# Kernel optimization log

Hardware: AMD Instinct MI355X
Metric: run time of the kernel (lower is better)

The kernel has to match this reference:

```python
import jax, jax.numpy as jnp
import numpy as np

N = 50000      # nodes
E = 800000     # edges (avg degree 16)
F_IN = 128     # input feature dim
HID = 128      # 2 * out_classes
OUT = 64       # out_classes


def setup_inputs() -> dict:
    key = jax.random.key(0)
    ks = jax.random.split(key, 12)
    x = jax.random.normal(ks[0], (N, F_IN), jnp.float32)
    edge_index = jax.random.randint(ks[1], (2, E), 0, N, jnp.int32)
    def lin(k, fi, fo):
        return jax.random.normal(k, (fi, fo), jnp.float32) / np.float32(np.sqrt(fi))
    return {
        "x": x,
        "edge_index": edge_index,
        "W1": lin(ks[2], F_IN, HID), "b1": jnp.zeros((HID,), jnp.float32),
        "W2": lin(ks[3], HID, HID),  "b2": jnp.zeros((HID,), jnp.float32),
        "W3": lin(ks[4], HID, HID),  "b3": jnp.zeros((HID,), jnp.float32),
        "jk_w": jax.random.normal(ks[5], (3,), jnp.float32),
        "fc_W": lin(ks[6], HID, OUT), "fc_b": jnp.zeros((OUT,), jnp.float32),
    }


def _gcn_conv(h, W, b, row, col, n):
    """PyG GCNConv: linear -> add self-loops -> sym-normalized aggregate -> bias."""
    h = h @ W                                        # [n, d_out]
    loops = jnp.arange(n, dtype=row.dtype)
    r = jnp.concatenate([row, loops])                # sources
    c = jnp.concatenate([col, loops])                # targets
    deg = jax.ops.segment_sum(jnp.ones_like(c, h.dtype), c, num_segments=n)
    dinv = jnp.where(deg > 0, jax.lax.rsqrt(deg), 0.0)
    norm = dinv[r] * dinv[c]                         # [E+n]
    msg = h[r] * norm[:, None]                       # gather + scale
    return jax.ops.segment_sum(msg, c, num_segments=n) + b


def _neighbor_mean(h, row, col, n):
    """sample_neighbors with scale_factor=2: exact mean over out-neighbors,
    own feature when degree == 0 (top-k branch is provably dead code)."""
    s = jax.ops.segment_sum(h[col], row, num_segments=n)
    deg = jax.ops.segment_sum(jnp.ones_like(row, h.dtype), row, num_segments=n)
    mean = s / jnp.maximum(deg, 1.0)[:, None]
    return jnp.where((deg > 0)[:, None], mean, h)


def reference(x, edge_index, W1, b1, W2, b2, W3, b3, jk_w, fc_W, fc_b):
    row, col = edge_index[0], edge_index[1]
    n = x.shape[0]
    # layer 0: GCN -> ReLU -> (dropout: eval identity) -> neighbor sampling
    h0 = jax.nn.relu(_gcn_conv(x, W1, b1, row, col, n))
    h0 = _neighbor_mean(h0, row, col, n)
    # layer 1: GCN -> ReLU; historical-activation update is identity on first call
    h1 = jax.nn.relu(_gcn_conv(h0, W2, b2, row, col, n))
    # layer 2
    h2 = jax.nn.relu(_gcn_conv(h1, W3, b3, row, col, n))
    # dynamic JK aggregation
    w = jax.nn.softmax(jk_w)
    h = w[0] * h0 + w[1] * h1 + w[2] * h2
    return h @ fc_W + fc_b
```

## Files before the change

kernel.cpp:

```cpp
#include <hip/hip_runtime.h>
#include <stdint.h>

typedef unsigned int  uint32;
typedef unsigned short u16;

typedef short bfx8 __attribute__((ext_vector_type(8)));
typedef float f32x4 __attribute__((ext_vector_type(4)));
typedef float f32x2 __attribute__((ext_vector_type(2)));

#define NBP 256
#define CH  2048

__device__ __forceinline__ float b2f(u16 u) {
    union { uint32 i; float f; } v; v.i = ((uint32)u) << 16; return v.f;
}
__device__ __forceinline__ u16 f2b(float f) {
    union { float f; uint32 i; } v; v.f = f;
    uint32 u = v.i;
    return (u16)((u + 0x7fffu + ((u >> 16) & 1u)) >> 16);
}
__device__ __forceinline__ float blo(uint32 u) {
    union { uint32 i; float f; } v; v.i = u << 16; return v.f;
}
__device__ __forceinline__ float bhi(uint32 u) {
    union { uint32 i; float f; } v; v.i = u & 0xffff0000u; return v.f;
}
__device__ __forceinline__ uint32 packbf(float a, float b) {
    return (uint32)f2b(a) | ((uint32)f2b(b) << 16);
}
__device__ __forceinline__ void splitf(float x, u16& h, u16& l) {
    h = f2b(x);
    l = f2b(x - b2f(h));
}
__device__ __forceinline__ void split8(const float* __restrict__ p, bfx8& hi, bfx8& lo) {
    f32x4 a = *(const f32x4*)p;
    f32x4 b = *(const f32x4*)(p + 4);
    float x[8] = {a[0], a[1], a[2], a[3], b[0], b[1], b[2], b[3]};
#pragma unroll
    for (int j = 0; j < 8; ++j) {
        u16 h, l; splitf(x[j], h, l);
        hi[j] = (short)h; lo[j] = (short)l;
    }
}

__global__ __launch_bounds__(256) void k_preA(
    const int* __restrict__ row, const int* __restrict__ col, int E, int Gh,
    int* __restrict__ cntC, int* __restrict__ cntR,
    const float* __restrict__ W1, const float* __restrict__ W2,
    const float* __restrict__ W3, const float* __restrict__ fcW,
    u16* __restrict__ WTh, u16* __restrict__ WTl, int WTN) {
    if ((int)blockIdx.x < Gh) {
        __shared__ int hp[NBP];
        int t = threadIdx.x;
        hp[t] = 0;
        __syncthreads();
        int base = blockIdx.x * CH;
        int n = E - base; if (n > CH) n = CH;
        for (int i = t; i < n; i += 256) {
            int r = row[base + i], c = col[base + i];
            atomicAdd(&hp[c >> 8], 1);
            atomicAdd(&hp[r >> 8], 0x10000);
        }
        __syncthreads();
        int v = hp[t];
        if (v & 0xffff) atomicAdd(&cntC[t], v & 0xffff);
        if (v >> 16)    atomicAdd(&cntR[t], v >> 16);
        return;
    }
    int i = ((int)blockIdx.x - Gh) * 256 + threadIdx.x;
    if (i >= WTN) return;
    float w;
    if (i < 3 * 16384) {
        int m = i >> 14, j = i & 16383;
        int fo = j >> 7, fi = j & 127;
        const float* W = (m == 0) ? W1 : (m == 1) ? W2 : W3;
        w = W[fi * 128 + fo];
    } else {
        int j = i - 3 * 16384;
        int fo = j >> 7, fi = j & 127;
        w = fcW[fi * 64 + fo];
    }
    u16 h, l; splitf(w, h, l);
    WTh[i] = h; WTl[i] = l;
}

__global__ __launch_bounds__(256) void k_scanB(
    const int* __restrict__ cntC, const int* __restrict__ cntR,
    int* __restrict__ bOffC, int* __restrict__ bOffR,
    int* __restrict__ curC, int* __restrict__ curR, int NB) {
    int t = threadIdx.x;
    int lane = t & 63, wid = t >> 6;
    __shared__ int wsum[4];
    for (int m = 0; m < 2; ++m) {
        const int* cnt = m ? cntR : cntC;
        int* bOff = m ? bOffR : bOffC;
        int* cur  = m ? curR  : curC;
        int v = (t < NB) ? cnt[t] : 0;
        int x = v;
#pragma unroll
        for (int d = 1; d < 64; d <<= 1) {
            int u = __shfl_up(x, d);
            if (lane >= d) x += u;
        }
        if (lane == 63) wsum[wid] = x;
        __syncthreads();
        int add = 0;
        for (int i = 0; i < wid; ++i) add += wsum[i];
        int ex = x + add - v;
        if (t <= NB) bOff[t] = ex;
        cur[t] = ex;
        __syncthreads();
    }
}

__device__ __forceinline__ void gemm128_f32_body(
    const float* __restrict__ A, const u16* __restrict__ WTh, const u16* __restrict__ WTl,
    const float* __restrict__ dinv, u16* __restrict__ G, int M, int blk) {
    const int lane = threadIdx.x & 63;
    const int q = lane >> 4, l = lane & 15;
    int rbase = blk * 128 + (threadIdx.x >> 6) * 32;
    if (rbase >= M) return;
    int r0 = rbase + l;      if (r0 >= M) r0 = M - 1;
    int r1 = rbase + 16 + l; if (r1 >= M) r1 = M - 1;

    f32x4 acc[2][8];
#pragma unroll
    for (int i = 0; i < 2; ++i)
#pragma unroll
        for (int j = 0; j < 8; ++j) acc[i][j] = (f32x4){0.f, 0.f, 0.f, 0.f};

#pragma unroll
    for (int kc = 0; kc < 4; ++kc) {
        int k0 = kc * 32 + q * 8;
        bfx8 ah0, al0, ah1, al1;
        split8(A + (size_t)r0 * 128 + k0, ah0, al0);
        split8(A + (size_t)r1 * 128 + k0, ah1, al1);
#pragma unroll
        for (int ct = 0; ct < 8; ++ct) {
            bfx8 bh = *(const bfx8*)(WTh + (ct * 16 + l) * 128 + k0);
            bfx8 bl = *(const bfx8*)(WTl + (ct * 16 + l) * 128 + k0);
            acc[0][ct] = __builtin_amdgcn_mfma_f32_16x16x32_bf16(ah0, bh, acc[0][ct], 0, 0, 0);
            acc[0][ct] = __builtin_amdgcn_mfma_f32_16x16x32_bf16(ah0, bl, acc[0][ct], 0, 0, 0);
            acc[0][ct] = __builtin_amdgcn_mfma_f32_16x16x32_bf16(al0, bh, acc[0][ct], 0, 0, 0);
            acc[1][ct] = __builtin_amdgcn_mfma_f32_16x16x32_bf16(ah1, bh, acc[1][ct], 0, 0, 0);
            acc[1][ct] = __builtin_amdgcn_mfma_f32_16x16x32_bf16(ah1, bl, acc[1][ct], 0, 0, 0);
            acc[1][ct] = __builtin_amdgcn_mfma_f32_16x16x32_bf16(al1, bh, acc[1][ct], 0, 0, 0);
        }
    }
#pragma unroll
    for (int rs = 0; rs < 2; ++rs) {
#pragma unroll
        for (int rr = 0; rr < 4; ++rr) {
            int rw = rbase + rs * 16 + q * 4 + rr;
            if (rw < M) {
                float dv = dinv ? dinv[rw] : 1.0f;
#pragma unroll
                for (int ct = 0; ct < 8; ++ct)
                    G[(size_t)rw * 128 + ct * 16 + l] = f2b(acc[rs][ct][rr] * dv);
            }
        }
    }
}

__global__ __launch_bounds__(256) void k_gemm0(
    const float* __restrict__ A, const u16* __restrict__ WTh, const u16* __restrict__ WTl,
    u16* __restrict__ G, int M) {
    gemm128_f32_body(A, WTh, WTl, nullptr, G, M, blockIdx.x);
}

__global__ __launch_bounds__(256) void k_gemm128_pl(
    const u16* __restrict__ Ah, const u16* __restrict__ Al,
    const u16* __restrict__ WTh, const u16* __restrict__ WTl,
    const float* __restrict__ dinv, u16* __restrict__ G, int M) {
    const int lane = threadIdx.x & 63;
    const int q = lane >> 4, l = lane & 15;
    int rbase = blockIdx.x * 128 + (threadIdx.x >> 6) * 32;
    if (rbase >= M) return;
    int r0 = rbase + l;      if (r0 >= M) r0 = M - 1;
    int r1 = rbase + 16 + l; if (r1 >= M) r1 = M - 1;

    f32x4 acc[2][8];
#pragma unroll
    for (int i = 0; i < 2; ++i)
#pragma unroll
        for (int j = 0; j < 8; ++j) acc[i][j] = (f32x4){0.f, 0.f, 0.f, 0.f};

#pragma unroll
    for (int kc = 0; kc < 4; ++kc) {
        int k0 = kc * 32 + q * 8;
        bfx8 ah0 = *(const bfx8*)(Ah + (size_t)r0 * 128 + k0);
        bfx8 al0 = *(const bfx8*)(Al + (size_t)r0 * 128 + k0);
        bfx8 ah1 = *(const bfx8*)(Ah + (size_t)r1 * 128 + k0);
        bfx8 al1 = *(const bfx8*)(Al + (size_t)r1 * 128 + k0);
#pragma unroll
        for (int ct = 0; ct < 8; ++ct) {
            bfx8 bh = *(const bfx8*)(WTh + (ct * 16 + l) * 128 + k0);
            bfx8 bl = *(const bfx8*)(WTl + (ct * 16 + l) * 128 + k0);
            acc[0][ct] = __builtin_amdgcn_mfma_f32_16x16x32_bf16(ah0, bh, acc[0][ct], 0, 0, 0);
            acc[0][ct] = __builtin_amdgcn_mfma_f32_16x16x32_bf16(ah0, bl, acc[0][ct], 0, 0, 0);
            acc[0][ct] = __builtin_amdgcn_mfma_f32_16x16x32_bf16(al0, bh, acc[0][ct], 0, 0, 0);
            acc[1][ct] = __builtin_amdgcn_mfma_f32_16x16x32_bf16(ah1, bh, acc[1][ct], 0, 0, 0);
            acc[1][ct] = __builtin_amdgcn_mfma_f32_16x16x32_bf16(ah1, bl, acc[1][ct], 0, 0, 0);
            acc[1][ct] = __builtin_amdgcn_mfma_f32_16x16x32_bf16(al1, bh, acc[1][ct], 0, 0, 0);
        }
    }
#pragma unroll
    for (int rs = 0; rs < 2; ++rs) {
#pragma unroll
        for (int rr = 0; rr < 4; ++rr) {
            int rw = rbase + rs * 16 + q * 4 + rr;
            if (rw < M) {
                float dv = dinv[rw];
#pragma unroll
                for (int ct = 0; ct < 8; ++ct)
                    G[(size_t)rw * 128 + ct * 16 + l] = f2b(acc[rs][ct][rr] * dv);
            }
        }
    }
}

__global__ __launch_bounds__(256) void k_partC(
    const int* __restrict__ row, const int* __restrict__ col, int E,
    int* __restrict__ curC, int* __restrict__ curR,
    uint32* __restrict__ partC, uint32* __restrict__ partR) {
    __shared__ uint32 stagedC[CH], stagedR[CH];
    __shared__ int hp[NBP], expk[NBP], curp[NBP], runC[NBP], runR[NBP];
    __shared__ int wsum[4];
    int t = threadIdx.x;
    int lane = t & 63, wid = t >> 6;
    int base = blockIdx.x * CH;
    int n = E - base; if (n > CH) n = CH;

    int er[8], ec[8];
#pragma unroll
    for (int j = 0; j < 8; ++j) {
        int i = t + j * 256;
        if (i < n) { er[j] = row[base + i]; ec[j] = col[base + i]; }
        else er[j] = -1;
    }
    hp[t] = 0;
    __syncthreads();
#pragma unroll
    for (int j = 0; j < 8; ++j) {
        if (er[j] >= 0) {
            atomicAdd(&hp[ec[j] >> 8], 1);
            atomicAdd(&hp[er[j] >> 8], 0x10000);
        }
    }
    __syncthreads();
    int v = hp[t];
    int x = v;
#pragma unroll
    for (int d = 1; d < 64; d <<= 1) {
        int u = __shfl_up(x, d);
        if (lane >= d) x += u;
    }
    if (lane == 63) wsum[wid] = x;
    __syncthreads();
    int add = 0;
    for (int i = 0; i < wid; ++i) add += wsum[i];
    int ex = x + add - v;
    expk[t] = ex;
    curp[t] = ex;
    int vC = v & 0xffff, vR = v >> 16;
    runC[t] = vC ? atomicAdd(&curC[t], vC) : 0;
    runR[t] = vR ? atomicAdd(&curR[t], vR) : 0;
    __syncthreads();
#pragma unroll
    for (int j = 0; j < 8; ++j) {
        if (er[j] >= 0) {
            int cb = ec[j] >> 8, rb = er[j] >> 8;
            int pC = atomicAdd(&curp[cb], 1) & 0xffff;
            stagedC[pC] = ((uint32)ec[j] << 16) | (uint32)er[j];
            int pR = atomicAdd(&curp[rb], 0x10000) >> 16;
            stagedR[pR] = ((uint32)er[j] << 16) | (uint32)ec[j];
        }
    }
    __syncthreads();
    for (int i = t; i < n; i += 256) {
        uint32 pv = stagedC[i];
        int b = pv >> 24;
        partC[runC[b] + (i - (expk[b] & 0xffff))] = pv;
    }
    for (int i = t; i < n; i += 256) {
        uint32 pv = stagedR[i];
        int b = pv >> 24;
        partR[runR[b] + (i - (expk[b] >> 16))] = pv;
    }
}

__global__ __launch_bounds__(256) void k_fillD(
    const uint32* __restrict__ partC, const uint32* __restrict__ partR,
    const int* __restrict__ bOffC, const int* __restrict__ bOffR,
    int* __restrict__ off_in, int* __restrict__ off_out,
    u16* __restrict__ csr_src, u16* __restrict__ csr_dst,
    float* __restrict__ dinv, int NB, int N, int E) {
    int part = ((int)blockIdx.x >= NB) ? 1 : 0;
    int b = (int)blockIdx.x - part * NB;
    const uint32* arr = part ? partR : partC;
    const int* bOff   = part ? bOffR : bOffC;
    int* offA         = part ? off_out : off_in;
    u16* csr          = part ? csr_dst : csr_src;
    int t = threadIdx.x;
    int lane = t & 63, wid = t >> 6;
    int base = bOff[b], end = bOff[b + 1];
    __shared__ int cnt[NBP], cur[NBP];
    __shared__ int wsum[4];
    cnt[t] = 0;
    __syncthreads();
    for (int i = base + t; i < end; i += 256)
        atomicAdd(&cnt[(arr[i] >> 16) & 255], 1);
    __syncthreads();
    int v = cnt[t];
    int x = v;
#pragma unroll
    for (int d = 1; d < 64; d <<= 1) {
        int u = __shfl_up(x, d);
        if (lane >= d) x += u;
    }
    if (lane == 63) wsum[wid] = x;
    __syncthreads();
    int add = 0;
    for (int i = 0; i < wid; ++i) add += wsum[i];
    int ex = x + add - v;
    cur[t] = ex;
    int node = (b << 8) + t;
    if (node < N) {
        offA[node] = base + ex;
        if (part == 0) dinv[node] = rsqrtf((float)(v + 1));
    }
    if (b == 0 && t == 0) offA[N] = E;
    __syncthreads();
    for (int i = base + t; i < end; i += 256) {
        uint32 pv = arr[i];
        int local = (pv >> 16) & 255;
        int pos = atomicAdd(&cur[local], 1);
        csr[base + pos] = (u16)(pv & 0xffffu);
    }
}

template <int MODE>
__global__ __launch_bounds__(256) void k_agg(
    const uint32* __restrict__ g, const u16* __restrict__ csr_src,
    const int* __restrict__ off, const float* __restrict__ dinv,
    const f32x2* __restrict__ bias, uint32* __restrict__ outH,
    uint32* __restrict__ outL, int n) {
    int w = (blockIdx.x * 256 + threadIdx.x) >> 6;
    if (w >= n) return;
    int lane = threadIdx.x & 63;
    float dc = dinv[w];
    uint32 sv = g[(size_t)w * 64 + lane];
    float s0, s1;
    if (MODE == 0) { s0 = blo(sv) * dc; s1 = bhi(sv) * dc; }
    else           { s0 = blo(sv);      s1 = bhi(sv); }
    int e = off[w], e1 = off[w + 1];
    for (; e + 8 <= e1; e += 8) {
        int ix[8];
#pragma unroll
        for (int j = 0; j < 8; ++j) ix[j] = csr_src[e + j];
        uint32 vv[8];
#pragma unroll
        for (int j = 0; j < 8; ++j) vv[j] = g[(size_t)ix[j] * 64 + lane];
        if (MODE == 0) {
            float dm[8];
#pragma unroll
            for (int j = 0; j < 8; ++j) dm[j] = dinv[ix[j]];
#pragma unroll
            for (int j = 0; j < 8; ++j) {
                s0 = fmaf(blo(vv[j]), dm[j], s0);
                s1 = fmaf(bhi(vv[j]), dm[j], s1);
            }
        } else {
#pragma unroll
            for (int j = 0; j < 8; ++j) { s0 += blo(vv[j]); s1 += bhi(vv[j]); }
        }
    }
    for (; e < e1; ++e) {
        int ix = csr_src[e];
        uint32 v = g[(size_t)ix * 64 + lane];
        if (MODE == 0) {
            float dm = dinv[ix];
            s0 = fmaf(blo(v), dm, s0);
            s1 = fmaf(bhi(v), dm, s1);
        } else {
            s0 += blo(v); s1 += bhi(v);
        }
    }
    f32x2 bb = bias[lane];
    float o0 = fmaxf(fmaf(s0, dc, bb[0]), 0.f);
    float o1 = fmaxf(fmaf(s1, dc, bb[1]), 0.f);
    if (MODE == 0) {
        outH[(size_t)w * 64 + lane] = packbf(o0, o1);
    } else {
        u16 h0, l0, h1, l1;
        splitf(o0, h0, l0);
        splitf(o1, h1, l1);
        outH[(size_t)w * 64 + lane] = (uint32)h0 | ((uint32)h1 << 16);
        outL[(size_t)w * 64 + lane] = (uint32)l0 | ((uint32)l1 << 16);
    }
}

__global__ __launch_bounds__(256) void k_mean(
    const uint32* __restrict__ h, const u16* __restrict__ csr_dst,
    const int* __restrict__ off, uint32* __restrict__ outH,
    uint32* __restrict__ outL, int n) {
    int w = (blockIdx.x * 256 + threadIdx.x) >> 6;
    if (w >= n) return;
    int lane = threadIdx.x & 63;
    int e = off[w], e1 = off[w + 1];
    int d = e1 - e;
    float s0 = 0.f, s1 = 0.f;
    for (; e + 8 <= e1; e += 8) {
        int ix[8];
#pragma unroll
        for (int j = 0; j < 8; ++j) ix[j] = csr_dst[e + j];
        uint32 vv[8];
#pragma unroll
        for (int j = 0; j < 8; ++j) vv[j] = h[(size_t)ix[j] * 64 + lane];
#pragma unroll
        for (int j = 0; j < 8; ++j) { s0 += blo(vv[j]); s1 += bhi(vv[j]); }
    }
    for (; e < e1; ++e) {
        uint32 v = h[(size_t)csr_dst[e] * 64 + lane];
        s0 += blo(v); s1 += bhi(v);
    }
    float o0, o1;
    if (d > 0) {
        float inv = 1.f / (float)d;
        o0 = s0 * inv; o1 = s1 * inv;
    } else {
        uint32 sv = h[(size_t)w * 64 + lane];
        o0 = blo(sv); o1 = bhi(sv);
    }
    u16 ha, la, hb, lb;
    splitf(o0, ha, la);
    splitf(o1, hb, lb);
    outH[(size_t)w * 64 + lane] = (uint32)ha | ((uint32)hb << 16);
    outL[(size_t)w * 64 + lane] = (uint32)la | ((uint32)lb << 16);
}

__global__ __launch_bounds__(256) void k_final(
    const u16* __restrict__ h0h, const u16* __restrict__ h0l,
    const u16* __restrict__ h1h, const u16* __restrict__ h1l,
    const u16* __restrict__ h2h, const u16* __restrict__ h2l,
    const float* __restrict__ jkw,
    const u16* __restrict__ fcWTh, const u16* __restrict__ fcWTl,
    const float* __restrict__ fcb, float* __restrict__ out, int M) {
    float a0 = jkw[0], a1 = jkw[1], a2 = jkw[2];
    float mx = fmaxf(a0, fmaxf(a1, a2));
    float e0 = expf(a0 - mx), e1 = expf(a1 - mx), e2 = expf(a2 - mx);
    float inv = 1.f / (e0 + e1 + e2);
    float w0 = e0 * inv, w1 = e1 * inv, w2 = e2 * inv;

    const int lane = threadIdx.x & 63;
    const int q = lane >> 4, l = lane & 15;
    int rbase = blockIdx.x * 128 + (threadIdx.x >> 6) * 32;
    if (rbase >= M) return;
    int r0 = rbase + l;      if (r0 >= M) r0 = M - 1;
    int r1 = rbase + 16 + l; if (r1 >= M) r1 = M - 1;

    f32x4 acc[2][4];
#pragma unroll
    for (int i = 0; i < 2; ++i)
#pragma unroll
        for (int j = 0; j < 4; ++j) acc[i][j] = (f32x4){0.f, 0.f, 0.f, 0.f};

    union U8 { bfx8 v; u16 u[8]; };

#pragma unroll
    for (int kc = 0; kc < 4; ++kc) {
        int k0 = kc * 32 + q * 8;
        bfx8 ah[2], al[2];
        const int rr2[2] = {r0, r1};
#pragma unroll
        for (int half = 0; half < 2; ++half) {
            size_t o = (size_t)rr2[half] * 128 + k0;
            U8 x0h, x0l, x1h, x1l, x2h, x2l, rh, rl;
            x0h.v = *(const bfx8*)(h0h + o); x0l.v = *(const bfx8*)(h0l + o);
            x1h.v = *(const bfx8*)(h1h + o); x1l.v = *(const bfx8*)(h1l + o);
            x2h.v = *(const bfx8*)(h2h + o); x2l.v = *(const bfx8*)(h2l + o);
#pragma unroll
            for (int j = 0; j < 8; ++j) {
                float v0 = b2f(x0h.u[j]) + b2f(x0l.u[j]);
                float v1 = b2f(x1h.u[j]) + b2f(x1l.u[j]);
                float v2 = b2f(x2h.u[j]) + b2f(x2l.u[j]);
                float c = w0 * v0 + w1 * v1 + w2 * v2;
                u16 ch, cl; splitf(c, ch, cl);
                rh.u[j] = ch; rl.u[j] = cl;
            }
            ah[half] = rh.v; al[half] = rl.v;
        }
#pragma unroll
        for (int ct = 0; ct < 4; ++ct) {
            bfx8 bh = *(const bfx8*)(fcWTh + (ct * 16 + l) * 128 + k0);
            bfx8 bl = *(const bfx8*)(fcWTl + (ct * 16 + l) * 128 + k0);
#pragma unroll
            for (int half = 0; half < 2; ++half) {
                acc[half][ct] = __builtin_amdgcn_mfma_f32_16x16x32_bf16(ah[half], bh, acc[half][ct], 0, 0, 0);
                acc[half][ct] = __builtin_amdgcn_mfma_f32_16x16x32_bf16(ah[half], bl, acc[half][ct], 0, 0, 0);
                acc[half][ct] = __builtin_amdgcn_mfma_f32_16x16x32_bf16(al[half], bh, acc[half][ct], 0, 0, 0);
            }
        }
    }
#pragma unroll
    for (int rs = 0; rs < 2; ++rs) {
#pragma unroll
        for (int rr = 0; rr < 4; ++rr) {
            int rw = rbase + rs * 16 + q * 4 + rr;
            if (rw < M) {
#pragma unroll
                for (int ct = 0; ct < 4; ++ct) {
                    int cc = ct * 16 + l;
                    out[(size_t)rw * 64 + cc] = acc[rs][ct][rr] + fcb[cc];
                }
            }
        }
    }
}

extern "C" void kernel_launch(void* const* d_in, const int* in_sizes, int n_in,
                              void* d_out, int out_size, void* d_ws, size_t ws_size,
                              hipStream_t stream) {
    const int N = in_sizes[0] / 128;
    const int E = in_sizes[1] / 2;
    const int NB = (N + 255) >> 8;

    const float* x    = (const float*)d_in[0];
    const int* row    = (const int*)d_in[1];
    const int* col    = row + E;
    const float* W1   = (const float*)d_in[2];
    const float* b1   = (const float*)d_in[3];
    const float* W2   = (const float*)d_in[4];
    const float* b2   = (const float*)d_in[5];
    const float* W3   = (const float*)d_in[6];
    const float* b3   = (const float*)d_in[7];
    const float* jkw  = (const float*)d_in[8];
    const float* fcW  = (const float*)d_in[9];
    const float* fcb  = (const float*)d_in[10];
    float* outp       = (float*)d_out;

    char* ws = (char*)d_ws;
    size_t off = 0;
    auto alloc = [&](size_t bytes) -> char* {
        char* p = ws + off;
        off += (bytes + 255) & ~(size_t)255;
        return p;
    };
    int* cntC   = (int*)alloc((size_t)2 * NBP * sizeof(int));
    int* cntR   = cntC + NBP;
    int* bOffC  = (int*)alloc((size_t)(NBP + 1) * sizeof(int));
    int* bOffR  = (int*)alloc((size_t)(NBP + 1) * sizeof(int));
    int* curC   = (int*)alloc((size_t)NBP * sizeof(int));
    int* curR   = (int*)alloc((size_t)NBP * sizeof(int));
    int* off_in  = (int*)alloc((size_t)(N + 1) * sizeof(int));
    int* off_out = (int*)alloc((size_t)(N + 1) * sizeof(int));
    uint32* partC = (uint32*)alloc((size_t)E * sizeof(uint32));
    uint32* partR = (uint32*)alloc((size_t)E * sizeof(uint32));
    u16* csr_src = (u16*)alloc((size_t)E * sizeof(u16));
    u16* csr_dst = (u16*)alloc((size_t)E * sizeof(u16));
    float* dinv  = (float*)alloc((size_t)N * sizeof(float));
    const int WTN = 3 * 16384 + 8192;
    u16* WTh = (u16*)alloc((size_t)WTN * sizeof(u16));
    u16* WTl = (u16*)alloc((size_t)WTN * sizeof(u16));
    size_t FB = (size_t)N * 128 * sizeof(u16);
    u16* gbuf = (u16*)alloc(FB);
    u16* t0   = (u16*)alloc(FB);
    u16* h0h = (u16*)alloc(FB); u16* h0l = (u16*)alloc(FB);
    u16* h1h = (u16*)alloc(FB); u16* h1l = (u16*)alloc(FB);
    u16* h2h = (u16*)alloc(FB); u16* h2l = (u16*)alloc(FB);

    hipMemsetAsync(cntC, 0, (size_t)2 * NBP * sizeof(int), stream);

    const int B = 256;
    int Gh = (E + CH - 1) / CH;
    int Gwt = (WTN + B - 1) / B;
    int Gg = (N + 127) / 128;
    k_preA<<<Gh + Gwt, B, 0, stream>>>(row, col, E, Gh, cntC, cntR,
                                       W1, W2, W3, fcW, WTh, WTl, WTN);
    k_scanB<<<1, B, 0, stream>>>(cntC, cntR, bOffC, bOffR, curC, curR, NB);
    k_gemm0<<<Gg, B, 0, stream>>>(x, WTh, WTl, gbuf, N);
    k_partC<<<Gh, B, 0, stream>>>(row, col, E, curC, curR, partC, partR);
    k_fillD<<<2 * NB, B, 0, stream>>>(partC, partR, bOffC, bOffR,
                                      off_in, off_out, csr_src, csr_dst, dinv, NB, N, E);

    int aggG = (N + 3) / 4;

    k_agg<0><<<aggG, B, 0, stream>>>((const uint32*)gbuf, csr_src, off_in, dinv,
                                     (const f32x2*)b1, (uint32*)t0, nullptr, N);
    k_mean<<<aggG, B, 0, stream>>>((const uint32*)t0, csr_dst, off_out,
                                   (uint32*)h0h, (uint32*)h0l, N);
    k_gemm128_pl<<<Gg, B, 0, stream>>>(h0h, h0l, WTh + 16384, WTl + 16384, dinv, gbuf, N);
    k_agg<1><<<aggG, B, 0, stream>>>((const uint32*)gbuf, csr_src, off_in, dinv,
                                     (const f32x2*)b2, (uint32*)h1h, (uint32*)h1l, N);
    k_gemm128_pl<<<Gg, B, 0, stream>>>(h1h, h1l, WTh + 2 * 16384, WTl + 2 * 16384, dinv, gbuf, N);
    k_agg<1><<<aggG, B, 0, stream>>>((const uint32*)gbuf, csr_src, off_in, dinv,
                                     (const f32x2*)b3, (uint32*)h2h, (uint32*)h2l, N);
    k_final<<<Gg, B, 0, stream>>>(h0h, h0l, h1h, h1l, h2h, h2l, jkw,
                                  WTh + 3 * 16384, WTl + 3 * 16384, fcb, outp, N);
}
```

Measured before the change: 381.4 us.

## Drop hi/lo activation split, use fixed-capacity buckets, widen gather unroll

```diff
diff --git a/kernel.cpp b/kernel.cpp
--- a/kernel.cpp
+++ b/kernel.cpp
@@ -10,6 +10,7 @@
 
 #define NBP 256
 #define CH  2048
+#define BS  4608
 
 __device__ __forceinline__ float b2f(u16 u) {
     union { uint32 i; float f; } v; v.i = ((uint32)u) << 16; return v.f;
@@ -43,31 +44,18 @@
     }
 }
 
-__global__ __launch_bounds__(256) void k_preA(
-    const int* __restrict__ row, const int* __restrict__ col, int E, int Gh,
-    int* __restrict__ cntC, int* __restrict__ cntR,
+__global__ __launch_bounds__(256) void k_init(
+    int* __restrict__ curC, int* __restrict__ curR,
     const float* __restrict__ W1, const float* __restrict__ W2,
     const float* __restrict__ W3, const float* __restrict__ fcW,
     u16* __restrict__ WTh, u16* __restrict__ WTl, int WTN) {
-    if ((int)blockIdx.x < Gh) {
-        __shared__ int hp[NBP];
-        int t = threadIdx.x;
-        hp[t] = 0;
-        __syncthreads();
-        int base = blockIdx.x * CH;
-        int n = E - base; if (n > CH) n = CH;
-        for (int i = t; i < n; i += 256) {
-            int r = row[base + i], c = col[base + i];
-            atomicAdd(&hp[c >> 8], 1);
-            atomicAdd(&hp[r >> 8], 0x10000);
-        }
-        __syncthreads();
-        int v = hp[t];
-        if (v & 0xffff) atomicAdd(&cntC[t], v & 0xffff);
-        if (v >> 16)    atomicAdd(&cntR[t], v >> 16);
+    int t = threadIdx.x;
+    if (blockIdx.x == 0) {
+        curC[t] = t * BS;
+        curR[t] = t * BS;
         return;
     }
-    int i = ((int)blockIdx.x - Gh) * 256 + threadIdx.x;
+    int i = ((int)blockIdx.x - 1) * 256 + t;
     if (i >= WTN) return;
     float w;
     if (i < 3 * 16384) {
@@ -84,41 +72,12 @@
     WTh[i] = h; WTl[i] = l;
 }
 
-__global__ __launch_bounds__(256) void k_scanB(
-    const int* __restrict__ cntC, const int* __restrict__ cntR,
-    int* __restrict__ bOffC, int* __restrict__ bOffR,
-    int* __restrict__ curC, int* __restrict__ curR, int NB) {
-    int t = threadIdx.x;
-    int lane = t & 63, wid = t >> 6;
-    __shared__ int wsum[4];
-    for (int m = 0; m < 2; ++m) {
-        const int* cnt = m ? cntR : cntC;
-        int* bOff = m ? bOffR : bOffC;
-        int* cur  = m ? curR  : curC;
-        int v = (t < NB) ? cnt[t] : 0;
-        int x = v;
-#pragma unroll
-        for (int d = 1; d < 64; d <<= 1) {
-            int u = __shfl_up(x, d);
-            if (lane >= d) x += u;
-        }
-        if (lane == 63) wsum[wid] = x;
-        __syncthreads();
-        int add = 0;
-        for (int i = 0; i < wid; ++i) add += wsum[i];
-        int ex = x + add - v;
-        if (t <= NB) bOff[t] = ex;
-        cur[t] = ex;
-        __syncthreads();
-    }
-}
-
-__device__ __forceinline__ void gemm128_f32_body(
+__global__ __launch_bounds__(256) void k_gemm0(
     const float* __restrict__ A, const u16* __restrict__ WTh, const u16* __restrict__ WTl,
-    const float* __restrict__ dinv, u16* __restrict__ G, int M, int blk) {
+    u16* __restrict__ G, int M) {
     const int lane = threadIdx.x & 63;
     const int q = lane >> 4, l = lane & 15;
-    int rbase = blk * 128 + (threadIdx.x >> 6) * 32;
+    int rbase = blockIdx.x * 128 + (threadIdx.x >> 6) * 32;
     if (rbase >= M) return;
     int r0 = rbase + l;      if (r0 >= M) r0 = M - 1;
     int r1 = rbase + 16 + l; if (r1 >= M) r1 = M - 1;
@@ -153,23 +112,16 @@
         for (int rr = 0; rr < 4; ++rr) {
             int rw = rbase + rs * 16 + q * 4 + rr;
             if (rw < M) {
-                float dv = dinv ? dinv[rw] : 1.0f;
 #pragma unroll
                 for (int ct = 0; ct < 8; ++ct)
-                    G[(size_t)rw * 128 + ct * 16 + l] = f2b(acc[rs][ct][rr] * dv);
-            }
-        }
-    }
-}
-
-__global__ __launch_bounds__(256) void k_gemm0(
-    const float* __restrict__ A, const u16* __restrict__ WTh, const u16* __restrict__ WTl,
-    u16* __restrict__ G, int M) {
-    gemm128_f32_body(A, WTh, WTl, nullptr, G, M, blockIdx.x);
-}
-
-__global__ __launch_bounds__(256) void k_gemm128_pl(
-    const u16* __restrict__ Ah, const u16* __restrict__ Al,
+                    G[(size_t)rw * 128 + ct * 16 + l] = f2b(acc[rs][ct][rr]);
+            }
+        }
+    }
+}
+
+__global__ __launch_bounds__(256) void k_gemm1p(
+    const u16* __restrict__ Ah,
     const u16* __restrict__ WTh, const u16* __restrict__ WTl,
     const float* __restrict__ dinv, u16* __restrict__ G, int M) {
     const int lane = threadIdx.x & 63;
@@ -189,19 +141,15 @@
     for (int kc = 0; kc < 4; ++kc) {
         int k0 = kc * 32 + q * 8;
         bfx8 ah0 = *(const bfx8*)(Ah + (size_t)r0 * 128 + k0);
-        bfx8 al0 = *(const bfx8*)(Al + (size_t)r0 * 128 + k0);
         bfx8 ah1 = *(const bfx8*)(Ah + (size_t)r1 * 128 + k0);
-        bfx8 al1 = *(const bfx8*)(Al + (size_t)r1 * 128 + k0);
 #pragma unroll
         for (int ct = 0; ct < 8; ++ct) {
             bfx8 bh = *(const bfx8*)(WTh + (ct * 16 + l) * 128 + k0);
             bfx8 bl = *(const bfx8*)(WTl + (ct * 16 + l) * 128 + k0);
             acc[0][ct] = __builtin_amdgcn_mfma_f32_16x16x32_bf16(ah0, bh, acc[0][ct], 0, 0, 0);
             acc[0][ct] = __builtin_amdgcn_mfma_f32_16x16x32_bf16(ah0, bl, acc[0][ct], 0, 0, 0);
-            acc[0][ct] = __builtin_amdgcn_mfma_f32_16x16x32_bf16(al0, bh, acc[0][ct], 0, 0, 0);
             acc[1][ct] = __builtin_amdgcn_mfma_f32_16x16x32_bf16(ah1, bh, acc[1][ct], 0, 0, 0);
             acc[1][ct] = __builtin_amdgcn_mfma_f32_16x16x32_bf16(ah1, bl, acc[1][ct], 0, 0, 0);
-            acc[1][ct] = __builtin_amdgcn_mfma_f32_16x16x32_bf16(al1, bh, acc[1][ct], 0, 0, 0);
         }
     }
 #pragma unroll
@@ -291,19 +239,21 @@
 
 __global__ __launch_bounds__(256) void k_fillD(
     const uint32* __restrict__ partC, const uint32* __restrict__ partR,
-    const int* __restrict__ bOffC, const int* __restrict__ bOffR,
-    int* __restrict__ off_in, int* __restrict__ off_out,
+    const int* __restrict__ curC, const int* __restrict__ curR,
+    int* __restrict__ off_in, int* __restrict__ end_in,
+    int* __restrict__ off_out, int* __restrict__ end_out,
     u16* __restrict__ csr_src, u16* __restrict__ csr_dst,
-    float* __restrict__ dinv, int NB, int N, int E) {
+    float* __restrict__ dinv, int NB, int N) {
     int part = ((int)blockIdx.x >= NB) ? 1 : 0;
     int b = (int)blockIdx.x - part * NB;
     const uint32* arr = part ? partR : partC;
-    const int* bOff   = part ? bOffR : bOffC;
+    const int* curA   = part ? curR : curC;
     int* offA         = part ? off_out : off_in;
+    int* endA         = part ? end_out : end_in;
     u16* csr          = part ? csr_dst : csr_src;
     int t = threadIdx.x;
     int lane = t & 63, wid = t >> 6;
-    int base = bOff[b], end = bOff[b + 1];
+    int base = b * BS, end = curA[b];
     __shared__ int cnt[NBP], cur[NBP];
     __shared__ int wsum[4];
     cnt[t] = 0;
@@ -327,9 +277,9 @@
     int node = (b << 8) + t;
     if (node < N) {
         offA[node] = base + ex;
+        endA[node] = base + ex + v;
         if (part == 0) dinv[node] = rsqrtf((float)(v + 1));
     }
-    if (b == 0 && t == 0) offA[N] = E;
     __syncthreads();
     for (int i = base + t; i < end; i += 256) {
         uint32 pv = arr[i];
@@ -342,9 +292,9 @@
 template <int MODE>
 __global__ __launch_bounds__(256) void k_agg(
     const uint32* __restrict__ g, const u16* __restrict__ csr_src,
-    const int* __restrict__ off, const float* __restrict__ dinv,
-    const f32x2* __restrict__ bias, uint32* __restrict__ outH,
-    uint32* __restrict__ outL, int n) {
+    const int* __restrict__ off, const int* __restrict__ endo,
+    const float* __restrict__ dinv,
+    const f32x2* __restrict__ bias, uint32* __restrict__ outH, int n) {
     int w = (blockIdx.x * 256 + threadIdx.x) >> 6;
     if (w >= n) return;
     int lane = threadIdx.x & 63;
@@ -353,26 +303,47 @@
     float s0, s1;
     if (MODE == 0) { s0 = blo(sv) * dc; s1 = bhi(sv) * dc; }
     else           { s0 = blo(sv);      s1 = bhi(sv); }
-    int e = off[w], e1 = off[w + 1];
-    for (; e + 8 <= e1; e += 8) {
-        int ix[8];
-#pragma unroll
-        for (int j = 0; j < 8; ++j) ix[j] = csr_src[e + j];
-        uint32 vv[8];
-#pragma unroll
-        for (int j = 0; j < 8; ++j) vv[j] = g[(size_t)ix[j] * 64 + lane];
+    int e = off[w], e1 = endo[w];
+    for (; e + 16 <= e1; e += 16) {
+        int ix[16];
+#pragma unroll
+        for (int j = 0; j < 16; ++j) ix[j] = csr_src[e + j];
+        uint32 vv[16];
+#pragma unroll
+        for (int j = 0; j < 16; ++j) vv[j] = g[(size_t)ix[j] * 64 + lane];
         if (MODE == 0) {
-            float dm[8];
-#pragma unroll
-            for (int j = 0; j < 8; ++j) dm[j] = dinv[ix[j]];
-#pragma unroll
-            for (int j = 0; j < 8; ++j) {
+            float dm[16];
+#pragma unroll
+            for (int j = 0; j < 16; ++j) dm[j] = dinv[ix[j]];
+#pragma unroll
+            for (int j = 0; j < 16; ++j) {
                 s0 = fmaf(blo(vv[j]), dm[j], s0);
                 s1 = fmaf(bhi(vv[j]), dm[j], s1);
             }
         } else {
 #pragma unroll
-            for (int j = 0; j < 8; ++j) { s0 += blo(vv[j]); s1 += bhi(vv[j]); }
+            for (int j = 0; j < 16; ++j) { s0 += blo(vv[j]); s1 += bhi(vv[j]); }
+        }
+    }
+    for (; e + 4 <= e1; e += 4) {
+        int ix[4];
+#pragma unroll
+        for (int j = 0; j < 4; ++j) ix[j] = csr_src[e + j];
+        uint32 vv[4];
+#pragma unroll
+        for (int j = 0; j < 4; ++j) vv[j] = g[(size_t)ix[j] * 64 + lane];
+        if (MODE == 0) {
+            float dm[4];
+#pragma unroll
+            for (int j = 0; j < 4; ++j) dm[j] = dinv[ix[j]];
+#pragma unroll
+            for (int j = 0; j < 4; ++j) {
+                s0 = fmaf(blo(vv[j]), dm[j], s0);
+                s1 = fmaf(bhi(vv[j]), dm[j], s1);
+            }
+        } else {
+#pragma unroll
+            for (int j = 0; j < 4; ++j) { s0 += blo(vv[j]); s1 += bhi(vv[j]); }
         }
     }
     for (; e < e1; ++e) {
@@ -389,36 +360,38 @@
     f32x2 bb = bias[lane];
     float o0 = fmaxf(fmaf(s0, dc, bb[0]), 0.f);
     float o1 = fmaxf(fmaf(s1, dc, bb[1]), 0.f);
-    if (MODE == 0) {
-        outH[(size_t)w * 64 + lane] = packbf(o0, o1);
-    } else {
-        u16 h0, l0, h1, l1;
-        splitf(o0, h0, l0);
-        splitf(o1, h1, l1);
-        outH[(size_t)w * 64 + lane] = (uint32)h0 | ((uint32)h1 << 16);
-        outL[(size_t)w * 64 + lane] = (uint32)l0 | ((uint32)l1 << 16);
-    }
+    outH[(size_t)w * 64 + lane] = packbf(o0, o1);
 }
 
 __global__ __launch_bounds__(256) void k_mean(
     const uint32* __restrict__ h, const u16* __restrict__ csr_dst,
-    const int* __restrict__ off, uint32* __restrict__ outH,
-    uint32* __restrict__ outL, int n) {
+    const int* __restrict__ off, const int* __restrict__ endo,
+    uint32* __restrict__ outH, int n) {
     int w = (blockIdx.x * 256 + threadIdx.x) >> 6;
     if (w >= n) return;
     int lane = threadIdx.x & 63;
-    int e = off[w], e1 = off[w + 1];
+    int e = off[w], e1 = endo[w];
     int d = e1 - e;
     float s0 = 0.f, s1 = 0.f;
-    for (; e + 8 <= e1; e += 8) {
-        int ix[8];
-#pragma unroll
-        for (int j = 0; j < 8; ++j) ix[j] = csr_dst[e + j];
-        uint32 vv[8];
-#pragma unroll
-        for (int j = 0; j < 8; ++j) vv[j] = h[(size_t)ix[j] * 64 + lane];
-#pragma unroll
-        for (int j = 0; j < 8; ++j) { s0 += blo(vv[j]); s1 += bhi(vv[j]); }
+    for (; e + 16 <= e1; e += 16) {
+        int ix[16];
+#pragma unroll
+        for (int j = 0; j < 16; ++j) ix[j] = csr_dst[e + j];
+        uint32 vv[16];
+#pragma unroll
+        for (int j = 0; j < 16; ++j) vv[j] = h[(size_t)ix[j] * 64 + lane];
+#pragma unroll
+        for (int j = 0; j < 16; ++j) { s0 += blo(vv[j]); s1 += bhi(vv[j]); }
+    }
+    for (; e + 4 <= e1; e += 4) {
+        int ix[4];
+#pragma unroll
+        for (int j = 0; j < 4; ++j) ix[j] = csr_dst[e + j];
+        uint32 vv[4];
+#pragma unroll
+        for (int j = 0; j < 4; ++j) vv[j] = h[(size_t)ix[j] * 64 + lane];
+#pragma unroll
+        for (int j = 0; j < 4; ++j) { s0 += blo(vv[j]); s1 += bhi(vv[j]); }
     }
     for (; e < e1; ++e) {
         uint32 v = h[(size_t)csr_dst[e] * 64 + lane];
@@ -432,18 +405,12 @@
         uint32 sv = h[(size_t)w * 64 + lane];
         o0 = blo(sv); o1 = bhi(sv);
     }
-    u16 ha, la, hb, lb;
-    splitf(o0, ha, la);
-    splitf(o1, hb, lb);
-    outH[(size_t)w * 64 + lane] = (uint32)ha | ((uint32)hb << 16);
-    outL[(size_t)w * 64 + lane] = (uint32)la | ((uint32)lb << 16);
+    outH[(size_t)w * 64 + lane] = packbf(o0, o1);
 }
 
 __global__ __launch_bounds__(256) void k_final(
-    const u16* __restrict__ h0h, const u16* __restrict__ h0l,
-    const u16* __restrict__ h1h, const u16* __restrict__ h1l,
-    const u16* __restrict__ h2h, const u16* __restrict__ h2l,
-    const float* __restrict__ jkw,
+    const u16* __restrict__ h0, const u16* __restrict__ h1,
+    const u16* __restrict__ h2, const float* __restrict__ jkw,
     const u16* __restrict__ fcWTh, const u16* __restrict__ fcWTl,
     const float* __restrict__ fcb, float* __restrict__ out, int M) {
     float a0 = jkw[0], a1 = jkw[1], a2 = jkw[2];
@@ -470,25 +437,21 @@
 #pragma unroll
     for (int kc = 0; kc < 4; ++kc) {
         int k0 = kc * 32 + q * 8;
-        bfx8 ah[2], al[2];
+        bfx8 ah[2];
         const int rr2[2] = {r0, r1};
 #pragma unroll
         for (int half = 0; half < 2; ++half) {
             size_t o = (size_t)rr2[half] * 128 + k0;
-            U8 x0h, x0l, x1h, x1l, x2h, x2l, rh, rl;
-            x0h.v = *(const bfx8*)(h0h + o); x0l.v = *(const bfx8*)(h0l + o);
-            x1h.v = *(const bfx8*)(h1h + o); x1l.v = *(const bfx8*)(h1l + o);
-            x2h.v = *(const bfx8*)(h2h + o); x2l.v = *(const bfx8*)(h2l + o);
+            U8 x0, x1, x2, rh;
+            x0.v = *(const bfx8*)(h0 + o);
+            x1.v = *(const bfx8*)(h1 + o);
+            x2.v = *(const bfx8*)(h2 + o);
 #pragma unroll
             for (int j = 0; j < 8; ++j) {
-                float v0 = b2f(x0h.u[j]) + b2f(x0l.u[j]);
-                float v1 = b2f(x1h.u[j]) + b2f(x1l.u[j]);
-                float v2 = b2f(x2h.u[j]) + b2f(x2l.u[j]);
-                float c = w0 * v0 + w1 * v1 + w2 * v2;
-                u16 ch, cl; splitf(c, ch, cl);
-                rh.u[j] = ch; rl.u[j] = cl;
-            }
-            ah[half] = rh.v; al[half] = rl.v;
+                float c = w0 * b2f(x0.u[j]) + w1 * b2f(x1.u[j]) + w2 * b2f(x2.u[j]);
+                rh.u[j] = f2b(c);
+            }
+            ah[half] = rh.v;
         }
 #pragma unroll
         for (int ct = 0; ct < 4; ++ct) {
@@ -498,7 +461,6 @@
             for (int half = 0; half < 2; ++half) {
                 acc[half][ct] = __builtin_amdgcn_mfma_f32_16x16x32_bf16(ah[half], bh, acc[half][ct], 0, 0, 0);
                 acc[half][ct] = __builtin_amdgcn_mfma_f32_16x16x32_bf16(ah[half], bl, acc[half][ct], 0, 0, 0);
-                acc[half][ct] = __builtin_amdgcn_mfma_f32_16x16x32_bf16(al[half], bh, acc[half][ct], 0, 0, 0);
             }
         }
     }
@@ -546,18 +508,16 @@
         off += (bytes + 255) & ~(size_t)255;
         return p;
     };
-    int* cntC   = (int*)alloc((size_t)2 * NBP * sizeof(int));
-    int* cntR   = cntC + NBP;
-    int* bOffC  = (int*)alloc((size_t)(NBP + 1) * sizeof(int));
-    int* bOffR  = (int*)alloc((size_t)(NBP + 1) * sizeof(int));
     int* curC   = (int*)alloc((size_t)NBP * sizeof(int));
     int* curR   = (int*)alloc((size_t)NBP * sizeof(int));
-    int* off_in  = (int*)alloc((size_t)(N + 1) * sizeof(int));
-    int* off_out = (int*)alloc((size_t)(N + 1) * sizeof(int));
-    uint32* partC = (uint32*)alloc((size_t)E * sizeof(uint32));
-    uint32* partR = (uint32*)alloc((size_t)E * sizeof(uint32));
-    u16* csr_src = (u16*)alloc((size_t)E * sizeof(u16));
-    u16* csr_dst = (u16*)alloc((size_t)E * sizeof(u16));
+    int* off_in  = (int*)alloc((size_t)N * sizeof(int));
+    int* end_in  = (int*)alloc((size_t)N * sizeof(int));
+    int* off_out = (int*)alloc((size_t)N * sizeof(int));
+    int* end_out = (int*)alloc((size_t)N * sizeof(int));
+    uint32* partC = (uint32*)alloc((size_t)NBP * BS * sizeof(uint32));
+    uint32* partR = (uint32*)alloc((size_t)NBP * BS * sizeof(uint32));
+    u16* csr_src = (u16*)alloc((size_t)NBP * BS * sizeof(u16));
+    u16* csr_dst = (u16*)alloc((size_t)NBP * BS * sizeof(u16));
     float* dinv  = (float*)alloc((size_t)N * sizeof(float));
     const int WTN = 3 * 16384 + 8192;
     u16* WTh = (u16*)alloc((size_t)WTN * sizeof(u16));
@@ -565,36 +525,34 @@
     size_t FB = (size_t)N * 128 * sizeof(u16);
     u16* gbuf = (u16*)alloc(FB);
     u16* t0   = (u16*)alloc(FB);
-    u16* h0h = (u16*)alloc(FB); u16* h0l = (u16*)alloc(FB);
-    u16* h1h = (u16*)alloc(FB); u16* h1l = (u16*)alloc(FB);
-    u16* h2h = (u16*)alloc(FB); u16* h2l = (u16*)alloc(FB);
-
-    hipMemsetAsync(cntC, 0, (size_t)2 * NBP * sizeof(int), stream);
+    u16* h0   = (u16*)alloc(FB);
+    u16* h1   = (u16*)alloc(FB);
+    u16* h2   = (u16*)alloc(FB);
 
     const int B = 256;
     int Gh = (E + CH - 1) / CH;
+    int Gg = (N + 127) / 128;
     int Gwt = (WTN + B - 1) / B;
-    int Gg = (N + 127) / 128;
-    k_preA<<<Gh + Gwt, B, 0, stream>>>(row, col, E, Gh, cntC, cntR,
-                                       W1, W2, W3, fcW, WTh, WTl, WTN);
-    k_scanB<<<1, B, 0, stream>>>(cntC, cntR, bOffC, bOffR, curC, curR, NB);
+
+    k_init<<<1 + Gwt, B, 0, stream>>>(curC, curR, W1, W2, W3, fcW, WTh, WTl, WTN);
     k_gemm0<<<Gg, B, 0, stream>>>(x, WTh, WTl, gbuf, N);
     k_partC<<<Gh, B, 0, stream>>>(row, col, E, curC, curR, partC, partR);
-    k_fillD<<<2 * NB, B, 0, stream>>>(partC, partR, bOffC, bOffR,
-                                      off_in, off_out, csr_src, csr_dst, dinv, NB, N, E);
+    k_fillD<<<2 * NB, B, 0, stream>>>(partC, partR, curC, curR,
+                                      off_in, end_in, off_out, end_out,
+                                      csr_src, csr_dst, dinv, NB, N);
 
     int aggG = (N + 3) / 4;
 
-    k_agg<0><<<aggG, B, 0, stream>>>((const uint32*)gbuf, csr_src, off_in, dinv,
-                                     (const f32x2*)b1, (uint32*)t0, nullptr, N);
-    k_mean<<<aggG, B, 0, stream>>>((const uint32*)t0, csr_dst, off_out,
-                                   (uint32*)h0h, (uint32*)h0l, N);
-    k_gemm128_pl<<<Gg, B, 0, stream>>>(h0h, h0l, WTh + 16384, WTl + 16384, dinv, gbuf, N);
-    k_agg<1><<<aggG, B, 0, stream>>>((const uint32*)gbuf, csr_src, off_in, dinv,
-                                     (const f32x2*)b2, (uint32*)h1h, (uint32*)h1l, N);
-    k_gemm128_pl<<<Gg, B, 0, stream>>>(h1h, h1l, WTh + 2 * 16384, WTl + 2 * 16384, dinv, gbuf, N);
-    k_agg<1><<<aggG, B, 0, stream>>>((const uint32*)gbuf, csr_src, off_in, dinv,
-                                     (const f32x2*)b3, (uint32*)h2h, (uint32*)h2l, N);
-    k_final<<<Gg, B, 0, stream>>>(h0h, h0l, h1h, h1l, h2h, h2l, jkw,
+    k_agg<0><<<aggG, B, 0, stream>>>((const uint32*)gbuf, csr_src, off_in, end_in, dinv,
+                                     (const f32x2*)b1, (uint32*)t0, N);
+    k_mean<<<aggG, B, 0, stream>>>((const uint32*)t0, csr_dst, off_out, end_out,
+                                   (uint32*)h0, N);
+    k_gemm1p<<<Gg, B, 0, stream>>>(h0, WTh + 16384, WTl + 16384, dinv, gbuf, N);
+    k_agg<1><<<aggG, B, 0, stream>>>((const uint32*)gbuf, csr_src, off_in, end_in, dinv,
+                                     (const f32x2*)b2, (uint32*)h1, N);
+    k_gemm1p<<<Gg, B, 0, stream>>>(h1, WTh + 2 * 16384, WTl + 2 * 16384, dinv, gbuf, N);
+    k_agg<1><<<aggG, B, 0, stream>>>((const uint32*)gbuf, csr_src, off_in, end_in, dinv,
+                                     (const f32x2*)b3, (uint32*)h2, N);
+    k_final<<<Gg, B, 0, stream>>>(h0, h1, h2, jkw,
                                   WTh + 3 * 16384, WTl + 3 * 16384, fcb, outp, N);
 }
```

Result: faster. 340.1 us (-10.8%).
